# Kernel tuning notes

Measured on AMD Instinct MI355X. Metric: run time of the kernel, lower is better.

The kernel has to match this reference:

```python
import jax, jax.numpy as jnp
import numpy as np

C = 64
K = 16
DEPTH = 4            # int(sqrt(K))
N_NODES = K - 1      # 15 internal nodes per subspace tree
D = 512              # input feature dim, D // C = 8 per subspace
M = 512              # output dim (LUT rows)
N = 16384            # number of input rows


def _make_selection_matrix(C, depth=DEPTH):
    # row i within a subspace selects the transformed dim used at tree level of node i
    lvl = [0, 1, 1, 2, 2, 2, 2, 3, 3, 3, 3, 3, 3, 3, 3]
    S = np.zeros((C * N_NODES, C * depth), np.float32)
    for c in range(C):
        for i in range(N_NODES):
            S[c * N_NODES + i, c * depth + lvl[i]] = 1.0
    return S


def _make_bit_matrix(C, K=K):
    # per-subspace (K, K-1) matrix: leaf k gets +/-1 on the 4 nodes along its root-to-leaf path
    Bm = np.zeros((K, N_NODES), np.float32)
    for k in range(K):
        node = 0
        for l in range(DEPTH):
            bit = (k >> (DEPTH - 1 - l)) & 1
            Bm[k, node] = 1.0 if bit else -1.0
            node = 2 * node + 1 + bit  # children of node i are 2i+1 (left) and 2i+2 (right)
    Bfull = np.zeros((C * K, C * N_NODES), np.float32)
    for c in range(C):
        Bfull[c * K:(c + 1) * K, c * N_NODES:(c + 1) * N_NODES] = Bm
    return Bfull


def setup_inputs() -> dict:
    key = jax.random.key(0)
    k1, k2, k3, k4 = jax.random.split(key, 4)
    I = jax.random.normal(k1, (N, D), dtype=jnp.float32)
    A = jax.random.normal(k2, (C, D // C, DEPTH), dtype=jnp.float32) * (1.0 / np.sqrt(D // C))
    T = jax.random.normal(k3, (C * N_NODES,), dtype=jnp.float32) * 0.1
    L = jax.random.normal(k4, (M, C, K), dtype=jnp.float32)
    S = jnp.asarray(_make_selection_matrix(C))
    B = jnp.asarray(_make_bit_matrix(C))
    return {"I": I, "A": A, "T": T, "L": L, "S": S, "B": B}


def reference(I, A, T, L, S, B):
    C_, sub, depth = A.shape
    Kq = L.shape[-1]
    n = I.shape[0]
    # block-diagonal per-subspace projection: (n, D) -> (n, C*depth)
    Ir = I.T.reshape(C_, sub, n)                      # (C, sub, n)
    xt = jnp.einsum('csn,csd->cdn', Ir, A)            # (C, depth, n)
    xt = xt.reshape(C_ * depth, n)                    # (C*depth, n)
    # tree encoding: per-node activations, tanh relaxation, leaf scores
    h = S @ xt - T[:, None]                           # (C*15, n)
    b = (B @ jnp.tanh(h)).reshape(C_, Kq, n)          # (C, K, n)
    # straight-through hard one-hot encoding with softmax backward
    E_soft = jax.nn.softmax(b, axis=1)
    E_hard = jax.nn.one_hot(jnp.argmax(b, axis=1), Kq, axis=1, dtype=b.dtype)
    E = E_hard + E_soft - jax.lax.stop_gradient(E_soft)  # (C, K, n)
    # LUT decode: out[n, m] = sum_c L[m, c, enc(n, c)]
    out = jnp.einsum('mck,ckn->nm', L, E)
    return out
```

## Files before the change

### kernel.cpp

```cpp
#include <hip/hip_runtime.h>
#include <hip/hip_fp16.h>
#include <math.h>

#define CC 64
#define KK 16
#define NNODES 15
#define DD 512
#define MM 512
#define NN 16384

typedef _Float16 half8 __attribute__((ext_vector_type(8)));
typedef float f32x4 __attribute__((ext_vector_type(4)));
typedef unsigned long long u64;

__device__ __forceinline__ float xla_tanhf(float x) {
    const float kMax = 7.90531110763549805f;
    bool tiny = fabsf(x) < 0.0004f;
    float xc = fminf(fmaxf(x, -kMax), kMax);
    float x2 = __fmul_rn(xc, xc);
    float p = __fmaf_rn(x2, -2.76076847742355e-16f, 2.00018790482477e-13f);
    p = __fmaf_rn(x2, p, -8.60467152213735e-11f);
    p = __fmaf_rn(x2, p, 5.12229709037114e-08f);
    p = __fmaf_rn(x2, p, 1.48572235717979e-05f);
    p = __fmaf_rn(x2, p, 6.37261928875436e-04f);
    p = __fmaf_rn(x2, p, 4.89352455891786e-03f);
    p = __fmul_rn(xc, p);
    float q = __fmaf_rn(x2, 1.19825839466702e-06f, 1.18534705686654e-04f);
    q = __fmaf_rn(x2, q, 2.26843463243900e-03f);
    q = __fmaf_rn(x2, q, 4.89352518554385e-03f);
    return tiny ? x : __fdiv_rn(p, q);
}

__global__ __launch_bounds__(256) void pack_bfrag(const float* __restrict__ L,
                                                  uint4* __restrict__ Bpk) {
    const int t    = blockIdx.x * 256 + threadIdx.x;
    const int lane = t & 63;
    const int mtg  = (t >> 6) & 31;
    const int ks   = t >> 11;
    const int kbase = ks * 32 + ((lane >> 4) << 3);
    const int c     = kbase >> 4;
    const int slot0 = kbase & 15;
    const int m     = (mtg << 4) + (lane & 15);

    const float* src = L + ((size_t)m * CC + c) * KK + slot0;
    float4 v0 = ((const float4*)src)[0];
    float4 v1 = ((const float4*)src)[1];
    union { half8 h; uint4 u; } pk;
    pk.h[0] = (_Float16)v0.x; pk.h[1] = (_Float16)v0.y;
    pk.h[2] = (_Float16)v0.z; pk.h[3] = (_Float16)v0.w;
    pk.h[4] = (_Float16)v1.x; pk.h[5] = (_Float16)v1.y;
    pk.h[6] = (_Float16)v1.z; pk.h[7] = (_Float16)v1.w;
    Bpk[t] = pk.u;
}

__global__ __launch_bounds__(256, 4) void encode_kernel(const float* __restrict__ I,
                                                        const float* __restrict__ A,
                                                        const float* __restrict__ T,
                                                        unsigned* __restrict__ codesG) {
    __shared__ float sA[32 * 64];
    __shared__ float sT[CC * NNODES];

    const int tid = threadIdx.x;
    for (int i = tid; i < CC * 32; i += 256) sA[(i & 31) * 64 + (i >> 5)] = A[i];
    for (int i = tid; i < CC * NNODES; i += 256) sT[i] = T[i];
    __syncthreads();

    const int lane = tid & 63;
    const int c    = lane;
    const int w    = ((blockIdx.x & 3) << 2) + (tid >> 6);
    const int tile = blockIdx.x >> 2;
    const int n0   = tile * 64;

    float a_[32];
#pragma unroll
    for (int i = 0; i < 32; ++i) a_[i] = sA[i * 64 + c];
    float tt[NNODES];
#pragma unroll
    for (int i = 0; i < NNODES; ++i) tt[i] = sT[c * NNODES + i];

    const int lvl[NNODES] = {0, 1, 1, 2, 2, 2, 2, 3, 3, 3, 3, 3, 3, 3, 3};
    unsigned codeWord = 0;
#pragma unroll 2
    for (int rr = 0; rr < 4; ++rr) {
        const int rl = (rr << 4) + w;
        const float* Ij = I + (size_t)(n0 + rl) * DD + c * 8;
        float4 v0 = ((const float4*)Ij)[0];
        float4 v1 = ((const float4*)Ij)[1];
        float iv[8] = {v0.x, v0.y, v0.z, v0.w, v1.x, v1.y, v1.z, v1.w};

        float t[4] = {0.f, 0.f, 0.f, 0.f};
#pragma unroll
        for (int s = 0; s < 8; ++s) {
            float v = iv[s];
#pragma unroll
            for (int d = 0; d < 4; ++d)
                t[d] = __fmaf_rn(v, a_[(s << 2) + d], t[d]);
        }

        float th[NNODES];
#pragma unroll
        for (int i = 0; i < NNODES; ++i) {
            float h = __fsub_rn(t[lvl[i]], tt[i]);
            th[i] = xla_tanhf(h);
        }

        int best = 0;
        float bestv = -3.0e38f;
#pragma unroll
        for (int k = 0; k < KK; ++k) {
            int node = 0;
            float s = 0.f;
#pragma unroll
            for (int l = 0; l < 4; ++l) {
                int bit = (k >> (3 - l)) & 1;
                s = __fadd_rn(s, bit ? th[node] : -th[node]);
                node = 2 * node + 1 + bit;
            }
            if (s > bestv) { bestv = s; best = k; }
        }
        codeWord |= ((unsigned)best) << (rr << 3);
    }
    codesG[(size_t)tile * 1024 + (w << 6) + c] = codeWord;
}

__global__ __launch_bounds__(256, 2) void decode_kernel(const unsigned* __restrict__ codesG,
                                                        const uint4* __restrict__ Bpk,
                                                        float* __restrict__ out) {
    __shared__ __align__(16) unsigned char sB[2][8192];
    __shared__ unsigned sCodes[2][16 * 68];

    const int tid = threadIdx.x;
    const int bn  = blockIdx.x >> 2;
    const int bm  = blockIdx.x & 3;
    const int n0  = bn << 7;
    const int m0  = bm << 7;

#pragma unroll
    for (int k = 0; k < 8; ++k) {
        int i = tid + (k << 8);
        sCodes[i >> 10][((i >> 6) & 15) * 68 + (i & 63)] = codesG[((size_t)bn << 11) + i];
    }

    const int w    = tid >> 6;
    const int lane = tid & 63;
    const int wn   = w >> 1;
    const int wm   = w & 1;
    const int r15  = lane & 15;
    const int sb   = ((lane >> 4) & 1) << 3;
    const int chi  = lane >> 5;

    const uint4* gA = Bpk + ((bm << 3) + w) * 64 + lane;
    const uint4* gB = gA + 4 * 64;

    __builtin_amdgcn_global_load_lds(
        (const __attribute__((address_space(1))) void*)gA,
        (__attribute__((address_space(3))) void*)&sB[0][w << 10], 16, 0, 0);
    __builtin_amdgcn_global_load_lds(
        (const __attribute__((address_space(1))) void*)gB,
        (__attribute__((address_space(3))) void*)&sB[0][(w + 4) << 10], 16, 0, 0);
    gA += 2048; gB += 2048;
    __syncthreads();

    f32x4 acc[4][4];
#pragma unroll
    for (int nt = 0; nt < 4; ++nt)
#pragma unroll
        for (int mt = 0; mt < 4; ++mt)
            acc[nt][mt] = (f32x4){0.f, 0.f, 0.f, 0.f};

    const unsigned* codeRow = &sCodes[wn][r15 * 68];
    const int bvoff = (wm << 2) << 10;

#pragma unroll 2
    for (int ks = 0; ks < 32; ++ks) {
        const int cur = ks & 1;
        if (ks < 31) {
            __builtin_amdgcn_global_load_lds(
                (const __attribute__((address_space(1))) void*)gA,
                (__attribute__((address_space(3))) void*)&sB[cur ^ 1][w << 10], 16, 0, 0);
            __builtin_amdgcn_global_load_lds(
                (const __attribute__((address_space(1))) void*)gB,
                (__attribute__((address_space(3))) void*)&sB[cur ^ 1][(w + 4) << 10], 16, 0, 0);
            gA += 2048; gB += 2048;
        }

        const unsigned cw = codeRow[(ks << 1) + chi];

        uint4 b[4];
#pragma unroll
        for (int j = 0; j < 4; ++j)
            b[j] = *(const uint4*)&sB[cur][bvoff + (j << 10) + (lane << 4)];

#pragma unroll
        for (int nt = 0; nt < 4; ++nt) {
            unsigned ud  = ((cw >> (nt << 3)) & 255u) - (unsigned)sb;
            unsigned ud2 = ud - 4u;
            u64 lo = (ud  < 4u) ? (0x3C00ull << ((ud  & 3u) << 4)) : 0ull;
            u64 hi = (ud2 < 4u) ? (0x3C00ull << ((ud2 & 3u) << 4)) : 0ull;
            union { u64 q[2]; half8 h; } uu; uu.q[0] = lo; uu.q[1] = hi;
#pragma unroll
            for (int mt = 0; mt < 4; ++mt) {
                union { uint4 u; half8 h; } bb; bb.u = b[mt];
                acc[nt][mt] = __builtin_amdgcn_mfma_f32_16x16x32_f16(uu.h, bb.h, acc[nt][mt], 0, 0, 0);
            }
        }

        __syncthreads();
    }

    const int rbase = (lane >> 4) << 2;
#pragma unroll
    for (int nt = 0; nt < 4; ++nt) {
#pragma unroll
        for (int r = 0; r < 4; ++r) {
            float* o = out + (size_t)(n0 + ((wn << 2) + nt) * 16 + rbase + r) * MM
                           + m0 + (wm << 6) + r15;
#pragma unroll
            for (int mt = 0; mt < 4; ++mt)
                o[mt << 4] = acc[nt][mt][r];
        }
    }
}

extern "C" void kernel_launch(void* const* d_in, const int* in_sizes, int n_in,
                              void* d_out, int out_size, void* d_ws, size_t ws_size,
                              hipStream_t stream) {
    const float* I = (const float*)d_in[0];
    const float* A = (const float*)d_in[1];
    const float* T = (const float*)d_in[2];
    const float* L = (const float*)d_in[3];

    uint4* Bpk = (uint4*)d_ws;
    unsigned* codesG = (unsigned*)((char*)d_ws + (1 << 20));
    float* out = (float*)d_out;

    hipLaunchKernelGGL(pack_bfrag, dim3(256), dim3(256), 0, stream, L, Bpk);
    hipLaunchKernelGGL(encode_kernel, dim3(1024), dim3(256), 0, stream, I, A, T, codesG);
    hipLaunchKernelGGL(decode_kernel, dim3(512), dim3(256), 0, stream, codesG, Bpk, out);
}
```

Baseline: 128.9 us.

## Replace LDS double-buffering in decode with register-prefetched direct global loads

The decode kernel no longer stages the packed LUT fragments and codes through shared memory with per-iteration barriers. Each wave loads its B fragments and code words straight from global memory into registers, using a four-deep rotating register prefetch so loads for upcoming k-steps are in flight while MFMAs run on the current one. This removes the LDS traffic and the __syncthreads per k-step, at the cost of more VGPRs and redundant global/L2 reads, since waves sharing fragments now fetch them separately.

```diff
diff --git a/kernel.cpp b/kernel.cpp
--- a/kernel.cpp
+++ b/kernel.cpp
@@ -123,23 +123,44 @@
     codesG[(size_t)tile * 1024 + (w << 6) + c] = codeWord;
 }
 
+#define LOADSET(S, ks_)                              \
+    b##S##0 = Bp[((ks_) * 32 + 0) * 64];             \
+    b##S##1 = Bp[((ks_) * 32 + 1) * 64];             \
+    b##S##2 = Bp[((ks_) * 32 + 2) * 64];             \
+    b##S##3 = Bp[((ks_) * 32 + 3) * 64];             \
+    c##S = cG[(ks_) << 1];
+
+#define COMPUTESET(S) do {                                                        \
+    const unsigned cw = c##S;                                                     \
+    half8 a_[4];                                                                  \
+    _Pragma("unroll")                                                             \
+    for (int nt = 0; nt < 4; ++nt) {                                              \
+        unsigned ud  = ((cw >> (nt << 3)) & 255u) - (unsigned)sb;                 \
+        unsigned ud2 = ud - 4u;                                                   \
+        u64 lo = (ud  < 4u) ? (0x3C00ull << ((ud  & 3u) << 4)) : 0ull;            \
+        u64 hi = (ud2 < 4u) ? (0x3C00ull << ((ud2 & 3u) << 4)) : 0ull;            \
+        union { u64 q[2]; half8 h; } uu; uu.q[0] = lo; uu.q[1] = hi;              \
+        a_[nt] = uu.h;                                                            \
+    }                                                                             \
+    union { uint4 u; half8 h; } q0, q1, q2, q3;                                   \
+    q0.u = b##S##0; q1.u = b##S##1; q2.u = b##S##2; q3.u = b##S##3;               \
+    _Pragma("unroll")                                                             \
+    for (int nt = 0; nt < 4; ++nt) {                                              \
+        acc[nt][0] = __builtin_amdgcn_mfma_f32_16x16x32_f16(a_[nt], q0.h, acc[nt][0], 0, 0, 0); \
+        acc[nt][1] = __builtin_amdgcn_mfma_f32_16x16x32_f16(a_[nt], q1.h, acc[nt][1], 0, 0, 0); \
+        acc[nt][2] = __builtin_amdgcn_mfma_f32_16x16x32_f16(a_[nt], q2.h, acc[nt][2], 0, 0, 0); \
+        acc[nt][3] = __builtin_amdgcn_mfma_f32_16x16x32_f16(a_[nt], q3.h, acc[nt][3], 0, 0, 0); \
+    }                                                                             \
+} while (0)
+
 __global__ __launch_bounds__(256, 2) void decode_kernel(const unsigned* __restrict__ codesG,
                                                         const uint4* __restrict__ Bpk,
                                                         float* __restrict__ out) {
-    __shared__ __align__(16) unsigned char sB[2][8192];
-    __shared__ unsigned sCodes[2][16 * 68];
-
     const int tid = threadIdx.x;
     const int bn  = blockIdx.x >> 2;
     const int bm  = blockIdx.x & 3;
     const int n0  = bn << 7;
     const int m0  = bm << 7;
-
-#pragma unroll
-    for (int k = 0; k < 8; ++k) {
-        int i = tid + (k << 8);
-        sCodes[i >> 10][((i >> 6) & 15) * 68 + (i & 63)] = codesG[((size_t)bn << 11) + i];
-    }
 
     const int w    = tid >> 6;
     const int lane = tid & 63;
@@ -149,17 +170,8 @@
     const int sb   = ((lane >> 4) & 1) << 3;
     const int chi  = lane >> 5;
 
-    const uint4* gA = Bpk + ((bm << 3) + w) * 64 + lane;
-    const uint4* gB = gA + 4 * 64;
-
-    __builtin_amdgcn_global_load_lds(
-        (const __attribute__((address_space(1))) void*)gA,
-        (__attribute__((address_space(3))) void*)&sB[0][w << 10], 16, 0, 0);
-    __builtin_amdgcn_global_load_lds(
-        (const __attribute__((address_space(1))) void*)gB,
-        (__attribute__((address_space(3))) void*)&sB[0][(w + 4) << 10], 16, 0, 0);
-    gA += 2048; gB += 2048;
-    __syncthreads();
+    const uint4* Bp = Bpk + ((bm << 3) + (wm << 2)) * 64 + lane;
+    const unsigned* cG = codesG + ((size_t)((bn << 1) | wn) << 10) + (r15 << 6) + chi;
 
     f32x4 acc[4][4];
 #pragma unroll
@@ -168,44 +180,24 @@
         for (int mt = 0; mt < 4; ++mt)
             acc[nt][mt] = (f32x4){0.f, 0.f, 0.f, 0.f};
 
-    const unsigned* codeRow = &sCodes[wn][r15 * 68];
-    const int bvoff = (wm << 2) << 10;
-
-#pragma unroll 2
-    for (int ks = 0; ks < 32; ++ks) {
-        const int cur = ks & 1;
-        if (ks < 31) {
-            __builtin_amdgcn_global_load_lds(
-                (const __attribute__((address_space(1))) void*)gA,
-                (__attribute__((address_space(3))) void*)&sB[cur ^ 1][w << 10], 16, 0, 0);
-            __builtin_amdgcn_global_load_lds(
-                (const __attribute__((address_space(1))) void*)gB,
-                (__attribute__((address_space(3))) void*)&sB[cur ^ 1][(w + 4) << 10], 16, 0, 0);
-            gA += 2048; gB += 2048;
-        }
-
-        const unsigned cw = codeRow[(ks << 1) + chi];
-
-        uint4 b[4];
-#pragma unroll
-        for (int j = 0; j < 4; ++j)
-            b[j] = *(const uint4*)&sB[cur][bvoff + (j << 10) + (lane << 4)];
-
-#pragma unroll
-        for (int nt = 0; nt < 4; ++nt) {
-            unsigned ud  = ((cw >> (nt << 3)) & 255u) - (unsigned)sb;
-            unsigned ud2 = ud - 4u;
-            u64 lo = (ud  < 4u) ? (0x3C00ull << ((ud  & 3u) << 4)) : 0ull;
-            u64 hi = (ud2 < 4u) ? (0x3C00ull << ((ud2 & 3u) << 4)) : 0ull;
-            union { u64 q[2]; half8 h; } uu; uu.q[0] = lo; uu.q[1] = hi;
-#pragma unroll
-            for (int mt = 0; mt < 4; ++mt) {
-                union { uint4 u; half8 h; } bb; bb.u = b[mt];
-                acc[nt][mt] = __builtin_amdgcn_mfma_f32_16x16x32_f16(uu.h, bb.h, acc[nt][mt], 0, 0, 0);
-            }
-        }
-
-        __syncthreads();
+    uint4 bA0, bA1, bA2, bA3; unsigned cA;
+    uint4 bB0, bB1, bB2, bB3; unsigned cB;
+    uint4 bC0, bC1, bC2, bC3; unsigned cC;
+    uint4 bD0, bD1, bD2, bD3; unsigned cD;
+
+    LOADSET(A, 0)
+    LOADSET(B, 1)
+    LOADSET(C, 2)
+    LOADSET(D, 3)
+
+#pragma unroll 1
+    for (int g = 0; g < 8; ++g) {
+        const int ks = g << 2;
+        const bool more = g < 7;
+        COMPUTESET(A); if (more) { LOADSET(A, ks + 4) }
+        COMPUTESET(B); if (more) { LOADSET(B, ks + 5) }
+        COMPUTESET(C); if (more) { LOADSET(C, ks + 6) }
+        COMPUTESET(D); if (more) { LOADSET(D, ks + 7) }
     }
 
     const int rbase = (lane >> 4) << 2;
```

New measurement: 123.3 us. -4.4%, faster.
